# Kernel optimization log

Measured on AMD Instinct MI355X. Metric: run time of the kernel, lower is better.

The kernel has to match this reference:

```python
import jax, jax.numpy as jnp
import numpy as np

B, N, D, C, Q = 8, 4096, 512, 1024, 8


def setup_inputs() -> dict:
    key = jax.random.key(0)
    k1, k2 = jax.random.split(key)
    x = jax.random.normal(k1, (B, N, D), dtype=jnp.float32)
    codebooks = jax.random.normal(k2, (Q, C, D), dtype=jnp.float32)
    return {"x": x, "codebooks": codebooks}


def reference(x, codebooks):
    """Residual VQ (Algorithm 1, SoundStream). Eval mode: no dropout, no implicit codebook.
    project_in / project_out are Identity since codebook_dim == dim.
    Each stage: nearest-code lookup (squared L2), straight-through quantize,
    residual subtraction (on detached quantized), accumulate quantized_out.
    """

    def step(carry, cb):  # cb: [C, D]
        residual, qout = carry
        # squared euclidean distances [B, N, C]: ||r||^2 - 2 r.e + ||e||^2
        d = (jnp.sum(residual * residual, axis=-1, keepdims=True)
             - 2.0 * jnp.einsum('bnd,cd->bnc', residual, cb)
             + jnp.sum(cb * cb, axis=-1))
        idx = jnp.argmin(d, axis=-1)            # [B, N]
        embed = cb[idx]                          # [B, N, D] gather
        # straight-through estimator (as in vector-quantize-pytorch VQ layer)
        quant = residual + jax.lax.stop_gradient(embed - residual)
        # commitment loss per stage: mse(quantize.detach(), input)
        loss = jnp.mean((jax.lax.stop_gradient(quant) - residual) ** 2)
        new_res = residual - jax.lax.stop_gradient(quant)
        return (new_res, qout + quant), (idx.astype(jnp.int32), loss)

    (_, qout), (indices, losses) = jax.lax.scan(
        step, (x, jnp.zeros_like(x)), codebooks)
    all_indices = jnp.moveaxis(indices, 0, -1)  # [B, N, Q]
    return qout, all_indices, losses
```

## Files before the change

### kernel.cpp

```cpp
#include <hip/hip_runtime.h>
#include <math.h>

#define B_   8
#define N_   4096
#define D_   512
#define C_   1024
#define Q_   8
#define ROWS (B_ * N_)

#define TAU  1.0f
#define RCH  8

typedef __attribute__((ext_vector_type(8))) short bf16x8;
typedef __attribute__((ext_vector_type(4))) float f32x4;

#define MF(a, b, c) __builtin_amdgcn_mfma_f32_16x16x32_bf16(a, b, c, 0, 0, 0)

__device__ __forceinline__ unsigned short bf16rn(float f) {
    unsigned int u = __builtin_bit_cast(unsigned int, f);
    return (unsigned short)((u + 0x7fffu + ((u >> 16) & 1u)) >> 16);
}
__device__ __forceinline__ int swzoff(int row, int q) {
    return row * 64 + ((q ^ ((row >> 1) & 3)) << 4);
}
__device__ __forceinline__ void gload16(const void* g, void* l) {
    __builtin_amdgcn_global_load_lds(
        (const __attribute__((address_space(1))) void*)g,
        (__attribute__((address_space(3))) void*)l, 16, 0, 0);
}

__global__ __launch_bounds__(256)
void conv_hi_kernel(const float* __restrict__ src, unsigned short* __restrict__ hi) {
    const int i4 = blockIdx.x * 256 + threadIdx.x;
    float4 v = ((const float4*)src)[i4];
    ushort4 h;
    h.x = bf16rn(v.x); h.y = bf16rn(v.y); h.z = bf16rn(v.z); h.w = bf16rn(v.w);
    ((ushort4*)hi)[i4] = h;
}

__global__ __launch_bounds__(256)
void code_norms_kernel(const float* __restrict__ cb, float* __restrict__ norms) {
    const int code = blockIdx.x * 4 + (threadIdx.x >> 6);
    const int lane = threadIdx.x & 63;
    const float* p = cb + (size_t)code * D_;
    float s = 0.f;
    #pragma unroll
    for (int d = lane * 4; d < D_; d += 256) {
        float4 v = *(const float4*)(p + d);
        s += v.x * v.x + v.y * v.y + v.z * v.z + v.w * v.w;
    }
    #pragma unroll
    for (int m = 1; m < 64; m <<= 1) s += __shfl_xor(s, m);
    if (lane == 0) norms[code] = s;
}

__global__ __launch_bounds__(256)
void cb_transpose_kernel(const float* __restrict__ cb, float* __restrict__ cbT) {
    __shared__ float tile[64][65];
    const int q = blockIdx.z;
    const int dBase = blockIdx.x * 64;
    const int cBase = blockIdx.y * 64;
    const int tc = threadIdx.x & 63;
    const int tr = threadIdx.x >> 6;
    const float* src = cb + (size_t)q * C_ * D_;
    float* dst = cbT + (size_t)q * D_ * C_;
    #pragma unroll
    for (int i = 0; i < 16; ++i) {
        const int c = tr + 4 * i;
        tile[c][tc] = src[(size_t)(cBase + c) * D_ + dBase + tc];
    }
    __syncthreads();
    #pragma unroll
    for (int i = 0; i < 16; ++i) {
        const int d = tr + 4 * i;
        dst[(size_t)(dBase + d) * C_ + cBase + tc] = tile[tc][d];
    }
}

__global__ __launch_bounds__(256, 2)
void rvq_gemm_pipe_kernel(const unsigned short* __restrict__ ahi,
                          const unsigned short* __restrict__ cbh,
                          const float* __restrict__ norms_s,
                          float* __restrict__ st_m1,
                          float* __restrict__ st_m2,
                          int* __restrict__ st_i1)
{
    __shared__ char lds[65536];

    const int tid  = threadIdx.x;
    const int lane = tid & 63;
    const int lc   = lane & 15;
    const int lq   = lane >> 4;
    const int wv   = tid >> 6;
    const int wr   = wv >> 1;
    const int wc   = wv & 1;
    const int rowBase = blockIdx.x * 128;
    const int half = blockIdx.y;

    const int srow = lane >> 2;
    const int qsw  = (lane & 3) ^ ((srow >> 1) & 3);

    const unsigned short* bsrc[8];
    int brow[8], isB[8], lof[8], ksub[8];
    #pragma unroll
    for (int i = 0; i < 8; ++i) {
        const int s   = wv * 8 + i;
        const int sub = s >> 4;
        const int b   = (s >> 3) & 1;
        const int j   = s & 7;
        bsrc[i] = b ? cbh : ahi;
        brow[i] = j * 16 + srow;
        isB[i]  = b;
        ksub[i] = sub * 32;
        lof[i]  = sub * 16384 + b * 8192 + j * 1024;
    }

    auto STAGE = [&](int db, int c, int kt) {
        char* lb = lds + db * 32768;
        #pragma unroll
        for (int i = 0; i < 8; ++i) {
            const int grow = (isB[i] ? (half * 512 + c * 128) : rowBase) + brow[i];
            gload16(bsrc[i] + (size_t)grow * D_ + kt * 64 + ksub[i] + qsw * 8,
                    lb + lof[i]);
        }
    };

    float c_m1 = INFINITY, c_m2 = INFINITY;
    int   c_i1 = 0;

    STAGE(0, 0, 0);
    __syncthreads();

    for (int chunk = 0; chunk < 4; ++chunk) {
        const int codeBase = half * 512 + chunk * 128;
        f32x4 acc[4][4];
        #pragma unroll
        for (int m = 0; m < 4; ++m)
            #pragma unroll
            for (int n = 0; n < 4; ++n) acc[m][n] = (f32x4){0.f, 0.f, 0.f, 0.f};

        for (int kt = 0; kt < 8; ++kt) {
            const int t  = chunk * 8 + kt;
            const int db = t & 1;
            if (t + 1 < 32)
                STAGE(db ^ 1, (t + 1) >> 3, (t + 1) & 7);

            #pragma unroll
            for (int sub = 0; sub < 2; ++sub) {
                char* base = lds + db * 32768 + sub * 16384;
                char* AhiB = base;
                char* BhiB = base + 8192;

                bf16x8 ah[4], bh[4];
                #pragma unroll
                for (int m = 0; m < 4; ++m) {
                    const int r = wr * 64 + m * 16 + lc;
                    ah[m] = *(const bf16x8*)(AhiB + swzoff(r, lq));
                }
                #pragma unroll
                for (int n = 0; n < 4; ++n) {
                    const int c = wc * 64 + n * 16 + lc;
                    bh[n] = *(const bf16x8*)(BhiB + swzoff(c, lq));
                }
                #pragma unroll
                for (int m = 0; m < 4; ++m)
                    #pragma unroll
                    for (int n = 0; n < 4; ++n)
                        acc[m][n] = MF(ah[m], bh[n], acc[m][n]);
            }
            __syncthreads();
        }

        const int cbase = codeBase + wc * 64;
        const float nrm0 = norms_s[cbase + lc];
        const float nrm1 = norms_s[cbase + 16 + lc];
        const float nrm2 = norms_s[cbase + 32 + lc];
        const float nrm3 = norms_s[cbase + 48 + lc];
        #pragma unroll
        for (int m = 0; m < 4; ++m) {
            #pragma unroll
            for (int r = 0; r < 4; ++r) {
                float s0 = fmaf(-2.f, acc[m][0][r], nrm0);
                float s1 = fmaf(-2.f, acc[m][1][r], nrm1);
                float s2 = fmaf(-2.f, acc[m][2][r], nrm2);
                float s3 = fmaf(-2.f, acc[m][3][r], nrm3);
                float m1 = s0, m2 = INFINITY;
                int   i1 = cbase + lc;
                if (s1 < m1) { m2 = m1; m1 = s1; i1 = cbase + 16 + lc; } else m2 = fminf(m2, s1);
                if (s2 < m1) { m2 = m1; m1 = s2; i1 = cbase + 32 + lc; } else m2 = fminf(m2, s2);
                if (s3 < m1) { m2 = m1; m1 = s3; i1 = cbase + 48 + lc; } else m2 = fminf(m2, s3);
                #pragma unroll
                for (int d = 1; d < 16; d <<= 1) {
                    float om1 = __shfl_xor(m1, d);
                    int   oi1 = __shfl_xor(i1, d);
                    float om2 = __shfl_xor(m2, d);
                    bool take = (om1 < m1) || (om1 == m1 && oi1 < i1);
                    float lose1 = take ? m1 : om1;
                    m2 = fminf(fminf(m2, om2), lose1);
                    m1 = take ? om1 : m1;
                    i1 = take ? oi1 : i1;
                }
                if (lc == (m * 4 + r)) {
                    bool take = (m1 < c_m1) || (m1 == c_m1 && i1 < c_i1);
                    float lose1 = take ? c_m1 : m1;
                    c_m2 = fminf(fminf(c_m2, m2), lose1);
                    c_m1 = take ? m1 : c_m1;
                    c_i1 = take ? i1 : c_i1;
                }
            }
        }
    }

    const int myrow = rowBase + wr * 64 + (lc >> 2) * 16 + lq * 4 + (lc & 3);
    const int quarter = half * 2 + wc;
    st_m1[quarter * ROWS + myrow] = c_m1;
    st_m2[quarter * ROWS + myrow] = c_m2;
    st_i1[quarter * ROWS + myrow] = c_i1;
}

__global__ __launch_bounds__(256, 2)
void rvq_gemm_fallback_kernel(const float* __restrict__ src,
                              const unsigned short* __restrict__ cbh,
                              const float* __restrict__ norms_s,
                              float* __restrict__ st_m1,
                              float* __restrict__ st_m2,
                              int* __restrict__ st_i1)
{
    __shared__ char lds[16384];
    char* AhiB = lds;
    char* BhiB = lds + 8192;

    const int tid  = threadIdx.x;
    const int lane = tid & 63;
    const int lc   = lane & 15;
    const int lq   = lane >> 4;
    const int wv   = tid >> 6;
    const int wr   = wv >> 1;
    const int wc   = wv & 1;
    const int rowBase = blockIdx.x * 128;
    const int half = blockIdx.y;

    float c_m1 = INFINITY, c_m2 = INFINITY;
    int   c_i1 = 0;

    const int arow  = tid >> 1;
    const int ahalf = tid & 1;

    for (int chunk = 0; chunk < 4; ++chunk) {
        const int codeBase = half * 512 + chunk * 128;
        f32x4 acc[4][4];
        #pragma unroll
        for (int m = 0; m < 4; ++m)
            #pragma unroll
            for (int n = 0; n < 4; ++n) acc[m][n] = (f32x4){0.f, 0.f, 0.f, 0.f};

        for (int kt = 0; kt < D_ / 32; ++kt) {
            __syncthreads();
            {
                const float* ap = src + (size_t)(rowBase + arow) * D_ + kt * 32 + ahalf * 16;
                float fv[16];
                *(float4*)&fv[0]  = ((const float4*)ap)[0];
                *(float4*)&fv[4]  = ((const float4*)ap)[1];
                *(float4*)&fv[8]  = ((const float4*)ap)[2];
                *(float4*)&fv[12] = ((const float4*)ap)[3];
                bf16x8 H0, H1;
                #pragma unroll
                for (int j = 0; j < 8; ++j) {
                    H0[j] = (short)bf16rn(fv[j]);
                    H1[j] = (short)bf16rn(fv[j + 8]);
                }
                const int q0 = ahalf * 2;
                *(bf16x8*)(AhiB + swzoff(arow, q0))     = H0;
                *(bf16x8*)(AhiB + swzoff(arow, q0 + 1)) = H1;
            }
            {
                const size_t boff = (size_t)(codeBase + arow) * D_ + kt * 32 + ahalf * 16;
                bf16x8 bh0 = *(const bf16x8*)(cbh + boff);
                bf16x8 bh1 = *(const bf16x8*)(cbh + boff + 8);
                const int q0 = ahalf * 2;
                *(bf16x8*)(BhiB + swzoff(arow, q0))     = bh0;
                *(bf16x8*)(BhiB + swzoff(arow, q0 + 1)) = bh1;
            }
            __syncthreads();
            bf16x8 ah[4], bh[4];
            #pragma unroll
            for (int m = 0; m < 4; ++m)
                ah[m] = *(const bf16x8*)(AhiB + swzoff(wr * 64 + m * 16 + lc, lq));
            #pragma unroll
            for (int n = 0; n < 4; ++n)
                bh[n] = *(const bf16x8*)(BhiB + swzoff(wc * 64 + n * 16 + lc, lq));
            #pragma unroll
            for (int m = 0; m < 4; ++m)
                #pragma unroll
                for (int n = 0; n < 4; ++n)
                    acc[m][n] = MF(ah[m], bh[n], acc[m][n]);
        }

        const int cbase = codeBase + wc * 64;
        const float nrm0 = norms_s[cbase + lc];
        const float nrm1 = norms_s[cbase + 16 + lc];
        const float nrm2 = norms_s[cbase + 32 + lc];
        const float nrm3 = norms_s[cbase + 48 + lc];
        #pragma unroll
        for (int m = 0; m < 4; ++m) {
            #pragma unroll
            for (int r = 0; r < 4; ++r) {
                float s0 = fmaf(-2.f, acc[m][0][r], nrm0);
                float s1 = fmaf(-2.f, acc[m][1][r], nrm1);
                float s2 = fmaf(-2.f, acc[m][2][r], nrm2);
                float s3 = fmaf(-2.f, acc[m][3][r], nrm3);
                float m1 = s0, m2 = INFINITY;
                int   i1 = cbase + lc;
                if (s1 < m1) { m2 = m1; m1 = s1; i1 = cbase + 16 + lc; } else m2 = fminf(m2, s1);
                if (s2 < m1) { m2 = m1; m1 = s2; i1 = cbase + 32 + lc; } else m2 = fminf(m2, s2);
                if (s3 < m1) { m2 = m1; m1 = s3; i1 = cbase + 48 + lc; } else m2 = fminf(m2, s3);
                #pragma unroll
                for (int d = 1; d < 16; d <<= 1) {
                    float om1 = __shfl_xor(m1, d);
                    int   oi1 = __shfl_xor(i1, d);
                    float om2 = __shfl_xor(m2, d);
                    bool take = (om1 < m1) || (om1 == m1 && oi1 < i1);
                    float lose1 = take ? m1 : om1;
                    m2 = fminf(fminf(m2, om2), lose1);
                    m1 = take ? om1 : m1;
                    i1 = take ? oi1 : i1;
                }
                if (lc == (m * 4 + r)) {
                    bool take = (m1 < c_m1) || (m1 == c_m1 && i1 < c_i1);
                    float lose1 = take ? c_m1 : m1;
                    c_m2 = fminf(fminf(c_m2, m2), lose1);
                    c_m1 = take ? m1 : c_m1;
                    c_i1 = take ? i1 : c_i1;
                }
            }
        }
    }

    const int myrow = rowBase + wr * 64 + (lc >> 2) * 16 + lq * 4 + (lc & 3);
    const int quarter = half * 2 + wc;
    st_m1[quarter * ROWS + myrow] = c_m1;
    st_m2[quarter * ROWS + myrow] = c_m2;
    st_i1[quarter * ROWS + myrow] = c_i1;
}

__global__ __launch_bounds__(256)
void merge_kernel(const float* __restrict__ st_m1, const float* __restrict__ st_m2,
                  const int* __restrict__ st_i1,
                  int* __restrict__ idx_i, float* __restrict__ idx_f,
                  int* __restrict__ list, int* __restrict__ nflag, int q) {
    const int row = blockIdx.x * 256 + threadIdx.x;
    float m1 = st_m1[row], m2 = st_m2[row];
    int   i1 = st_i1[row];
    #pragma unroll
    for (int qt = 1; qt < 4; ++qt) {
        float om1 = st_m1[qt * ROWS + row];
        float om2 = st_m2[qt * ROWS + row];
        int   oi1 = st_i1[qt * ROWS + row];
        if (om1 < m1) { m2 = fminf(m1, om2); m1 = om1; i1 = oi1; }
        else          { m2 = fminf(m2, om1); }
    }
    idx_i[row] = i1;
    idx_f[(size_t)row * Q_ + q] = (float)i1;
    if (m2 - m1 < TAU) {
        const int p = atomicAdd(nflag, 1);
        list[p] = row;
    }
}

__global__ __launch_bounds__(256)
void rescue_par_kernel(const float* __restrict__ src, const float* __restrict__ cbT_s,
                       const float* __restrict__ norms_s,
                       const int* __restrict__ list, const int* __restrict__ nflag_p,
                       unsigned long long* __restrict__ pk)
{
    __shared__ float As[D_][RCH];
    __shared__ int   rows_s[RCH];
    const int nflag = nflag_p[0];
    const int nitems = ((nflag + RCH - 1) / RCH) * 4;
    const int tid  = threadIdx.x;
    const int lane = tid & 63;

    for (int item = blockIdx.x; item < nitems; item += gridDim.x) {
        const int chunk   = item >> 2;
        const int quarter = item & 3;
        __syncthreads();
        if (tid < RCH) {
            const int li = chunk * RCH + tid;
            rows_s[tid] = list[li < nflag ? li : nflag - 1];
        }
        __syncthreads();
        #pragma unroll
        for (int i = 0; i < 4; ++i) {
            const int v  = tid + 256 * i;
            const int r  = v >> 7;
            const int k4 = (v & 127) * 4;
            float4 f = *(const float4*)(src + (size_t)rows_s[r] * D_ + k4);
            As[k4 + 0][r] = f.x; As[k4 + 1][r] = f.y;
            As[k4 + 2][r] = f.z; As[k4 + 3][r] = f.w;
        }
        __syncthreads();

        const int code = quarter * 256 + tid;
        const float* ct = cbT_s + code;
        float acc[RCH];
        #pragma unroll
        for (int r = 0; r < RCH; ++r) acc[r] = 0.f;

        float pa[8], pb[8];
        #pragma unroll
        for (int e = 0; e < 8; ++e) pa[e] = ct[(size_t)e * C_];
        for (int k = 0; k < D_; k += 16) {
            #pragma unroll
            for (int e = 0; e < 8; ++e) pb[e] = ct[(size_t)(k + 8 + e) * C_];
            #pragma unroll
            for (int e = 0; e < 8; ++e)
                #pragma unroll
                for (int r = 0; r < RCH; ++r)
                    acc[r] = fmaf(pa[e], As[k + e][r], acc[r]);
            if (k + 16 < D_) {
                #pragma unroll
                for (int e = 0; e < 8; ++e) pa[e] = ct[(size_t)(k + 16 + e) * C_];
            }
            #pragma unroll
            for (int e = 0; e < 8; ++e)
                #pragma unroll
                for (int r = 0; r < RCH; ++r)
                    acc[r] = fmaf(pb[e], As[k + 8 + e][r], acc[r]);
        }

        const float nr = norms_s[code];
        #pragma unroll
        for (int r = 0; r < RCH; ++r) {
            const float s = fmaf(-2.f, acc[r], nr);
            unsigned int u = __builtin_bit_cast(unsigned int, s);
            unsigned int ord = (u & 0x80000000u) ? ~u : (u | 0x80000000u);
            unsigned long long p =
                ((unsigned long long)ord << 32) | (unsigned int)code;
            #pragma unroll
            for (int d = 1; d < 64; d <<= 1) {
                unsigned long long o = __shfl_xor(p, d);
                p = (o < p) ? o : p;
            }
            if (lane == 0) {
                const int li = chunk * RCH + r;
                if (li < nflag)
                    atomicMin(&pk[rows_s[r]], p);
            }
        }
    }
}

__global__ __launch_bounds__(256)
void rescue_unpack_kernel(const unsigned long long* __restrict__ pk,
                          const int* __restrict__ list,
                          const int* __restrict__ nflag_p,
                          int* __restrict__ idx_i, float* __restrict__ idx_f, int q)
{
    const int nflag = nflag_p[0];
    for (int i = blockIdx.x * 256 + threadIdx.x; i < nflag; i += gridDim.x * 256) {
        const int row  = list[i];
        const int code = (int)(pk[row] & 0xFFFFFFFFull);
        idx_i[row] = code;
        idx_f[(size_t)row * Q_ + q] = (float)code;
    }
}

#define FMA_HALF(v0, v1, v2, v3, kk)                                  \
    {                                                                 \
        _Pragma("unroll")                                             \
        for (int e = 0; e < 4; ++e) {                                 \
            const float b0e = ((const float*)&(v0))[e];               \
            const float b1e = ((const float*)&(v1))[e];               \
            const float b2e = ((const float*)&(v2))[e];               \
            const float b3e = ((const float*)&(v3))[e];               \
            _Pragma("unroll")                                         \
            for (int r = 0; r < RCH; ++r) {                           \
                const float a = As[(kk) + e][r];                      \
                acc[0][r] = fmaf(b0e, a, acc[0][r]);                  \
                acc[1][r] = fmaf(b1e, a, acc[1][r]);                  \
                acc[2][r] = fmaf(b2e, a, acc[2][r]);                  \
                acc[3][r] = fmaf(b3e, a, acc[3][r]);                  \
            }                                                         \
        }                                                             \
    }

__global__ __launch_bounds__(256)
void rescue_kernel(const float* __restrict__ src, const float* __restrict__ cb,
                   const float* __restrict__ norms_s,
                   const int* __restrict__ list, const int* __restrict__ nflag_p,
                   int* __restrict__ idx_i, float* __restrict__ idx_f, int q)
{
    __shared__ float As[D_][RCH];
    __shared__ int   rows_s[RCH];
    __shared__ float wm[4][RCH];
    __shared__ int   wi[4][RCH];
    const int nflag = nflag_p[0];
    const int tid = threadIdx.x;

    const float* const c0 = cb + (size_t)(tid      ) * D_;
    const float* const c1 = cb + (size_t)(tid + 256) * D_;
    const float* const c2 = cb + (size_t)(tid + 512) * D_;
    const float* const c3 = cb + (size_t)(tid + 768) * D_;

    for (int chunk = blockIdx.x; chunk * RCH < nflag; chunk += gridDim.x) {
        __syncthreads();
        if (tid < RCH) {
            const int li = chunk * RCH + tid;
            rows_s[tid] = list[li < nflag ? li : nflag - 1];
        }
        __syncthreads();
        #pragma unroll
        for (int i = 0; i < 4; ++i) {
            const int v  = tid + 256 * i;
            const int r  = v >> 7;
            const int k4 = (v & 127) * 4;
            float4 f = *(const float4*)(src + (size_t)rows_s[r] * D_ + k4);
            As[k4 + 0][r] = f.x; As[k4 + 1][r] = f.y;
            As[k4 + 2][r] = f.z; As[k4 + 3][r] = f.w;
        }
        __syncthreads();

        float acc[4][RCH];
        #pragma unroll
        for (int j = 0; j < 4; ++j)
            #pragma unroll
            for (int r = 0; r < RCH; ++r) acc[j][r] = 0.f;

        float4 pa0 = *(const float4*)(c0);
        float4 pa1 = *(const float4*)(c1);
        float4 pa2 = *(const float4*)(c2);
        float4 pa3 = *(const float4*)(c3);
        for (int k = 0; k < D_; k += 8) {
            float4 pb0 = *(const float4*)(c0 + k + 4);
            float4 pb1 = *(const float4*)(c1 + k + 4);
            float4 pb2 = *(const float4*)(c2 + k + 4);
            float4 pb3 = *(const float4*)(c3 + k + 4);
            FMA_HALF(pa0, pa1, pa2, pa3, k);
            if (k + 8 < D_) {
                pa0 = *(const float4*)(c0 + k + 8);
                pa1 = *(const float4*)(c1 + k + 8);
                pa2 = *(const float4*)(c2 + k + 8);
                pa3 = *(const float4*)(c3 + k + 8);
            }
            FMA_HALF(pb0, pb1, pb2, pb3, k + 4);
        }

        float m1[RCH]; int i1[RCH];
        #pragma unroll
        for (int r = 0; r < RCH; ++r) { m1[r] = INFINITY; i1[r] = 0; }
        #pragma unroll
        for (int j = 0; j < 4; ++j) {
            const int c = tid + 256 * j;
            const float nr = norms_s[c];
            #pragma unroll
            for (int r = 0; r < RCH; ++r) {
                const float s = fmaf(-2.f, acc[j][r], nr);
                if (s < m1[r]) { m1[r] = s; i1[r] = c; }
            }
        }
        #pragma unroll
        for (int d = 1; d < 64; d <<= 1)
            #pragma unroll
            for (int r = 0; r < RCH; ++r) {
                const float om = __shfl_xor(m1[r], d);
                const int   oi = __shfl_xor(i1[r], d);
                if (om < m1[r] || (om == m1[r] && oi < i1[r])) { m1[r] = om; i1[r] = oi; }
            }
        if ((tid & 63) == 0)
            #pragma unroll
            for (int r = 0; r < RCH; ++r) { wm[tid >> 6][r] = m1[r]; wi[tid >> 6][r] = i1[r]; }
        __syncthreads();
        if (tid < RCH) {
            float bm = wm[0][tid]; int bi = wi[0][tid];
            #pragma unroll
            for (int w = 1; w < 4; ++w)
                if (wm[w][tid] < bm || (wm[w][tid] == bm && wi[w][tid] < bi)) {
                    bm = wm[w][tid]; bi = wi[w][tid];
                }
            const int li = chunk * RCH + tid;
            if (li < nflag) {
                const int row = rows_s[tid];
                idx_i[row] = bi;
                idx_f[(size_t)row * Q_ + q] = (float)bi;
            }
        }
    }
}

__global__ __launch_bounds__(256)
void update_kernel(const float* __restrict__ src, float* __restrict__ dst,
                   const float* __restrict__ x, const float* __restrict__ cb,
                   const int* __restrict__ idx_i, float* __restrict__ loss_out,
                   unsigned short* __restrict__ rhi,
                   int is_last, int write_hl) {
    __shared__ int ids[64];
    const int tid = threadIdx.x;
    const int rowBase = blockIdx.x * 64;
    if (tid < 64) ids[tid] = idx_i[rowBase + tid];
    __syncthreads();
    float lsum = 0.f;
    #pragma unroll 4
    for (int e4 = tid; e4 < 64 * D_ / 4; e4 += 256) {
        const int row  = e4 >> 7;
        const int d    = (e4 & 127) * 4;
        const int code = ids[row];
        const size_t off = (size_t)(rowBase + row) * D_ + d;
        float4 r = *(const float4*)(src + off);
        float4 e = *(const float4*)(cb + (size_t)code * D_ + d);
        float4 nr = make_float4(r.x - e.x, r.y - e.y, r.z - e.z, r.w - e.w);
        lsum += nr.x * nr.x + nr.y * nr.y + nr.z * nr.z + nr.w * nr.w;
        if (is_last) {
            float4 xv = *(const float4*)(x + off);
            *(float4*)(dst + off) = make_float4(xv.x - nr.x, xv.y - nr.y,
                                                xv.z - nr.z, xv.w - nr.w);
        } else {
            *(float4*)(dst + off) = nr;
        }
        if (write_hl) {
            ushort4 h;
            h.x = bf16rn(nr.x);
            h.y = bf16rn(nr.y);
            h.z = bf16rn(nr.z);
            h.w = bf16rn(nr.w);
            *(ushort4*)(rhi + off) = h;
        }
    }
    #pragma unroll
    for (int m = 1; m < 64; m <<= 1) lsum += __shfl_xor(lsum, m);
    if ((tid & 63) == 0)
        atomicAdd(loss_out, lsum * (1.0f / ((float)ROWS * (float)D_)));
}

extern "C" void kernel_launch(void* const* d_in, const int* in_sizes, int n_in,
                              void* d_out, int out_size, void* d_ws, size_t ws_size,
                              hipStream_t stream) {
    const float* x  = (const float*)d_in[0];
    const float* cb = (const float*)d_in[1];

    float* qout   = (float*)d_out;
    float* idx_f  = (float*)d_out + (size_t)ROWS * D_;
    float* losses = idx_f + (size_t)ROWS * Q_;

    char* w = (char*)d_ws;
    unsigned short* cb_hi = (unsigned short*)w;
    float* cbT = (float*)(cb_hi + (size_t)Q_ * C_ * D_);
    float* norms = cbT + (size_t)Q_ * C_ * D_;
    float* st_m1 = norms + Q_ * C_;
    float* st_m2 = st_m1 + 4 * ROWS;
    int*   st_i1 = (int*)(st_m2 + 4 * ROWS);
    int*   idx_i = st_i1 + 4 * ROWS;
    int*   list  = idx_i + ROWS;
    int*   nflag = list + ROWS;
    unsigned long long* pk = (unsigned long long*)(nflag + 64);
    unsigned short* res_hi = (unsigned short*)(pk + ROWS);

    const size_t need = (size_t)((char*)(res_hi + (size_t)ROWS * D_) - w);
    const int preconv = (ws_size >= need) ? 1 : 0;

    hipMemsetAsync(losses, 0, Q_ * sizeof(float), stream);
    hipMemsetAsync(nflag, 0, 8 * sizeof(int), stream);
    conv_hi_kernel<<<Q_ * C_ * D_ / 1024, 256, 0, stream>>>(cb, cb_hi);
    code_norms_kernel<<<Q_ * C_ / 4, 256, 0, stream>>>(cb, norms);
    if (preconv) {
        conv_hi_kernel<<<(int)((size_t)ROWS * D_ / 1024), 256, 0, stream>>>(x, res_hi);
        cb_transpose_kernel<<<dim3(D_ / 64, C_ / 64, Q_), 256, 0, stream>>>(cb, cbT);
    }

    for (int q = 0; q < Q_; ++q) {
        const float* src = (q == 0) ? x : qout;
        const float* cb_s = cb + (size_t)q * C_ * D_;
        if (preconv)
            rvq_gemm_pipe_kernel<<<dim3(ROWS / 128, 2), 256, 0, stream>>>(
                res_hi, cb_hi + (size_t)q * C_ * D_,
                norms + (size_t)q * C_, st_m1, st_m2, st_i1);
        else
            rvq_gemm_fallback_kernel<<<dim3(ROWS / 128, 2), 256, 0, stream>>>(
                src, cb_hi + (size_t)q * C_ * D_,
                norms + (size_t)q * C_, st_m1, st_m2, st_i1);
        merge_kernel<<<ROWS / 256, 256, 0, stream>>>(
            st_m1, st_m2, st_i1, idx_i, idx_f, list, nflag + q, q);
        if (preconv) {
            hipMemsetAsync(pk, 0xFF, (size_t)ROWS * sizeof(unsigned long long), stream);
            rescue_par_kernel<<<1024, 256, 0, stream>>>(
                src, cbT + (size_t)q * D_ * C_, norms + (size_t)q * C_,
                list, nflag + q, pk);
            rescue_unpack_kernel<<<64, 256, 0, stream>>>(
                pk, list, nflag + q, idx_i, idx_f, q);
        } else {
            rescue_kernel<<<256, 256, 0, stream>>>(
                src, cb_s, norms + (size_t)q * C_, list, nflag + q, idx_i, idx_f, q);
        }
        update_kernel<<<ROWS / 64, 256, 0, stream>>>(
            src, qout, x, cb_s, idx_i, losses + q, res_hi,
            (q == Q_ - 1) ? 1 : 0, (preconv && q < Q_ - 1) ? 1 : 0);
    }
}
```

Before: 1.399 ms.

## Keep full residual row tile resident in LDS and stream codebook chunks

The GEMM kernel now loads a 64-row residual tile (all 512 dims) into LDS once and loops over all 1024 codes in 8 chunks, double-buffering only codebook tiles. Each wave covers 32 codes by 64 rows, so there are four quarter partial results per row instead of split halves across blocks. This removes repeated residual loads per K step and the grid split over code halves. In exchange LDS use grows to 96KB, which limits occupancy to one block per CU, and each MFMA step has a smaller tile of 4x2.

```diff
diff --git a/kernel.cpp b/kernel.cpp
--- a/kernel.cpp
+++ b/kernel.cpp
@@ -85,110 +85,92 @@
                           float* __restrict__ st_m2,
                           int* __restrict__ st_i1)
 {
-    __shared__ char lds[65536];
+    __shared__ char lds[98304];
+    char* const ldsA = lds;
+    char* const ldsB = lds + 65536;
 
     const int tid  = threadIdx.x;
     const int lane = tid & 63;
     const int lc   = lane & 15;
     const int lq   = lane >> 4;
     const int wv   = tid >> 6;
-    const int wr   = wv >> 1;
-    const int wc   = wv & 1;
-    const int rowBase = blockIdx.x * 128;
-    const int half = blockIdx.y;
+    const int rowBase = blockIdx.x * 64;
 
     const int srow = lane >> 2;
     const int qsw  = (lane & 3) ^ ((srow >> 1) & 3);
 
-    const unsigned short* bsrc[8];
-    int brow[8], isB[8], lof[8], ksub[8];
     #pragma unroll
-    for (int i = 0; i < 8; ++i) {
-        const int s   = wv * 8 + i;
-        const int sub = s >> 4;
-        const int b   = (s >> 3) & 1;
-        const int j   = s & 7;
-        bsrc[i] = b ? cbh : ahi;
-        brow[i] = j * 16 + srow;
-        isB[i]  = b;
-        ksub[i] = sub * 32;
-        lof[i]  = sub * 16384 + b * 8192 + j * 1024;
-    }
-
-    auto STAGE = [&](int db, int c, int kt) {
-        char* lb = lds + db * 32768;
-        #pragma unroll
-        for (int i = 0; i < 8; ++i) {
-            const int grow = (isB[i] ? (half * 512 + c * 128) : rowBase) + brow[i];
-            gload16(bsrc[i] + (size_t)grow * D_ + kt * 64 + ksub[i] + qsw * 8,
-                    lb + lof[i]);
+    for (int i = 0; i < 16; ++i) {
+        const int s    = wv * 16 + i;
+        const int kt32 = s >> 2;
+        const int j    = s & 3;
+        gload16(ahi + (size_t)(rowBase + j * 16 + srow) * D_ + kt32 * 32 + qsw * 8,
+                ldsA + kt32 * 4096 + j * 1024);
+    }
+
+    auto STAGE_B = [&](int db, int c, int kt) {
+        #pragma unroll
+        for (int i = 0; i < 4; ++i) {
+            const int s   = wv * 4 + i;
+            const int sub = s >> 3;
+            const int j   = s & 7;
+            gload16(cbh + (size_t)(c * 128 + j * 16 + srow) * D_ + kt * 64 + sub * 32 + qsw * 8,
+                    ldsB + db * 16384 + sub * 8192 + j * 1024);
         }
     };
 
     float c_m1 = INFINITY, c_m2 = INFINITY;
     int   c_i1 = 0;
 
-    STAGE(0, 0, 0);
+    STAGE_B(0, 0, 0);
     __syncthreads();
 
-    for (int chunk = 0; chunk < 4; ++chunk) {
-        const int codeBase = half * 512 + chunk * 128;
-        f32x4 acc[4][4];
+    for (int chunk = 0; chunk < 8; ++chunk) {
+        f32x4 acc[4][2];
         #pragma unroll
         for (int m = 0; m < 4; ++m)
             #pragma unroll
-            for (int n = 0; n < 4; ++n) acc[m][n] = (f32x4){0.f, 0.f, 0.f, 0.f};
+            for (int n = 0; n < 2; ++n) acc[m][n] = (f32x4){0.f, 0.f, 0.f, 0.f};
 
         for (int kt = 0; kt < 8; ++kt) {
             const int t  = chunk * 8 + kt;
             const int db = t & 1;
-            if (t + 1 < 32)
-                STAGE(db ^ 1, (t + 1) >> 3, (t + 1) & 7);
+            if (t + 1 < 64)
+                STAGE_B(db ^ 1, (t + 1) >> 3, (t + 1) & 7);
 
             #pragma unroll
             for (int sub = 0; sub < 2; ++sub) {
-                char* base = lds + db * 32768 + sub * 16384;
-                char* AhiB = base;
-                char* BhiB = base + 8192;
-
-                bf16x8 ah[4], bh[4];
-                #pragma unroll
-                for (int m = 0; m < 4; ++m) {
-                    const int r = wr * 64 + m * 16 + lc;
-                    ah[m] = *(const bf16x8*)(AhiB + swzoff(r, lq));
-                }
-                #pragma unroll
-                for (int n = 0; n < 4; ++n) {
-                    const int c = wc * 64 + n * 16 + lc;
-                    bh[n] = *(const bf16x8*)(BhiB + swzoff(c, lq));
-                }
+                char* AhiB = ldsA + (kt * 2 + sub) * 4096;
+                char* BhiB = ldsB + db * 16384 + sub * 8192;
+
+                bf16x8 ah[4], bh[2];
+                #pragma unroll
+                for (int m = 0; m < 4; ++m)
+                    ah[m] = *(const bf16x8*)(AhiB + swzoff(m * 16 + lc, lq));
+                #pragma unroll
+                for (int n = 0; n < 2; ++n)
+                    bh[n] = *(const bf16x8*)(BhiB + swzoff(wv * 32 + n * 16 + lc, lq));
                 #pragma unroll
                 for (int m = 0; m < 4; ++m)
                     #pragma unroll
-                    for (int n = 0; n < 4; ++n)
+                    for (int n = 0; n < 2; ++n)
                         acc[m][n] = MF(ah[m], bh[n], acc[m][n]);
             }
             __syncthreads();
         }
 
-        const int cbase = codeBase + wc * 64;
+        const int cbase = chunk * 128 + wv * 32;
         const float nrm0 = norms_s[cbase + lc];
         const float nrm1 = norms_s[cbase + 16 + lc];
-        const float nrm2 = norms_s[cbase + 32 + lc];
-        const float nrm3 = norms_s[cbase + 48 + lc];
         #pragma unroll
         for (int m = 0; m < 4; ++m) {
             #pragma unroll
             for (int r = 0; r < 4; ++r) {
                 float s0 = fmaf(-2.f, acc[m][0][r], nrm0);
                 float s1 = fmaf(-2.f, acc[m][1][r], nrm1);
-                float s2 = fmaf(-2.f, acc[m][2][r], nrm2);
-                float s3 = fmaf(-2.f, acc[m][3][r], nrm3);
                 float m1 = s0, m2 = INFINITY;
                 int   i1 = cbase + lc;
                 if (s1 < m1) { m2 = m1; m1 = s1; i1 = cbase + 16 + lc; } else m2 = fminf(m2, s1);
-                if (s2 < m1) { m2 = m1; m1 = s2; i1 = cbase + 32 + lc; } else m2 = fminf(m2, s2);
-                if (s3 < m1) { m2 = m1; m1 = s3; i1 = cbase + 48 + lc; } else m2 = fminf(m2, s3);
                 #pragma unroll
                 for (int d = 1; d < 16; d <<= 1) {
                     float om1 = __shfl_xor(m1, d);
@@ -211,8 +193,8 @@
         }
     }
 
-    const int myrow = rowBase + wr * 64 + (lc >> 2) * 16 + lq * 4 + (lc & 3);
-    const int quarter = half * 2 + wc;
+    const int myrow = rowBase + (lc >> 2) * 16 + lq * 4 + (lc & 3);
+    const int quarter = wv;
     st_m1[quarter * ROWS + myrow] = c_m1;
     st_m2[quarter * ROWS + myrow] = c_m2;
     st_i1[quarter * ROWS + myrow] = c_i1;
@@ -670,7 +652,7 @@
         const float* src = (q == 0) ? x : qout;
         const float* cb_s = cb + (size_t)q * C_ * D_;
         if (preconv)
-            rvq_gemm_pipe_kernel<<<dim3(ROWS / 128, 2), 256, 0, stream>>>(
+            rvq_gemm_pipe_kernel<<<ROWS / 64, 256, 0, stream>>>(
                 res_hi, cb_hi + (size_t)q * C_ * D_,
                 norms + (size_t)q * C_, st_m1, st_m2, st_i1);
         else
```

Result: slower. 2.099 ms (+50.0%).
